# Performance work log

Hardware: AMD Instinct MI355X
Metric: run time of the kernel (lower is better)

The kernel has to match this reference:

```python
import jax, jax.numpy as jnp
import numpy as np

B, S, E, H = 2, 2048, 1024, 16
D = E // H


def setup_inputs() -> dict:
    key = jax.random.key(0)
    ks = jax.random.split(key, 12)
    init = lambda k, shp: (jax.random.normal(k, shp, dtype=jnp.float32) * 0.02)
    return {
        "q": jax.random.normal(ks[0], (B, S, E), dtype=jnp.float32),
        "k": jax.random.normal(ks[1], (B, S, E), dtype=jnp.float32),
        "v": jax.random.normal(ks[2], (B, S, E), dtype=jnp.float32),
        "wq": init(ks[3], (E, E)), "bq": jnp.zeros((E,), jnp.float32),
        "wk": init(ks[4], (E, E)), "bk": jnp.zeros((E,), jnp.float32),
        "wv": init(ks[5], (E, E)), "bv": jnp.zeros((E,), jnp.float32),
        "wo": init(ks[6], (E, E)), "bo": jnp.zeros((E,), jnp.float32),
        "gamma": jnp.ones((E,), jnp.float32),
        "beta": jnp.zeros((E,), jnp.float32),
        "mask": 1,
    }


def _split_heads(x):
    # [B,S,E] -> [B,H,S,D]
    return x.reshape(x.shape[0], x.shape[1], H, D).transpose(0, 2, 1, 3)


def _mha(q, k, v, wq, bq, wk, bk, wv, bv, wo, bo, gamma, beta, causal):
    residual = q
    query = _split_heads(q @ wq + bq)
    key = _split_heads(k @ wk + bk)
    value = _split_heads(v @ wv + bv)
    scale = jnp.sqrt(jnp.float32(D)) + 1e-8  # matches torch: sqrt(dk) + 1e-8
    score = jnp.einsum("bhqd,bhkd->bhqk", query, key) / scale
    if causal:
        cm = jnp.tril(jnp.ones((S, S), dtype=bool))  # 1 - triu(...,1)
        score = jnp.where(cm[None, None], score, -jnp.inf)
    attn = jax.nn.softmax(score, axis=-1)
    ctx = jnp.einsum("bhqk,bhkd->bhqd", attn, value)
    ctx = ctx.transpose(0, 2, 1, 3).reshape(ctx.shape[0], S, E)
    o = ctx @ wo + bo  # dropout is identity in eval mode
    x = residual + o
    mu = jnp.mean(x, axis=-1, keepdims=True)
    var = jnp.var(x, axis=-1, keepdims=True)
    return (x - mu) / jnp.sqrt(var + 1e-5) * gamma + beta


def reference(q, k, v, wq, bq, wk, bk, wv, bv, wo, bo, gamma, beta, mask):
    return _mha(q, k, v, wq, bq, wk, bk, wv, bv, wo, bo, gamma, beta, bool(mask))
```

## Files before the change

### kernel.cpp

```cpp
#include <hip/hip_runtime.h>
#include <hip/hip_bf16.h>

typedef __bf16 bf16x8 __attribute__((ext_vector_type(8)));
typedef __attribute__((ext_vector_type(8))) short short8_t;
typedef __attribute__((ext_vector_type(4))) short short4_t;
typedef __attribute__((ext_vector_type(4))) float f32x4;

#define DEV __device__ __forceinline__

constexpr int Bc = 2, Sc = 2048, Ec = 1024, Hc = 16, Dc = 64;
constexpr int Mc = Bc * Sc;
constexpr int NT = Sc / 64;
constexpr float kQS = (float)((1.0 / (8.0 + 1e-8)) * 1.4426950408889634);

DEV short f2bf(float f) {
  unsigned int u = __builtin_bit_cast(unsigned int, f);
  unsigned int r = u + 0x7fffu + ((u >> 16) & 1u);
  return (short)(r >> 16);
}
DEV short bfc(float f) { __bf16 h = (__bf16)f; return __builtin_bit_cast(short, h); }

DEV float fexp2(float x) {
#if __has_builtin(__builtin_amdgcn_exp2f)
  return __builtin_amdgcn_exp2f(x);
#else
  float r;
  asm("v_exp_f32 %0, %1" : "=v"(r) : "v"(x));
  return r;
#endif
}

DEV void gload16(const short* g, short* lds) {
  __builtin_amdgcn_global_load_lds((const __attribute__((address_space(1))) void*)g,
                                   (__attribute__((address_space(3))) void*)lds, 16, 0, 0);
}

struct Prep {
  const float* w[4]; short* wt[4];
  const float* x[3]; short* y[3];
};
__global__ __launch_bounds__(256) void k_prep(Prep a) {
  const int bid = blockIdx.x;
  if (bid < 4096) {
    __shared__ float tile[32][33];
    const int z = bid >> 10, bk = (bid >> 5) & 31, bn = bid & 31;
    const float* w = a.w[z];
    short* wt = a.wt[z];
    int tx = threadIdx.x & 31, ty = threadIdx.x >> 5;
#pragma unroll
    for (int i = 0; i < 4; i++)
      tile[ty + i * 8][tx] = w[(size_t)(bk * 32 + ty + i * 8) * Ec + bn * 32 + tx];
    __syncthreads();
#pragma unroll
    for (int i = 0; i < 4; i++)
      wt[(size_t)(bn * 32 + ty + i * 8) * Ec + bk * 32 + tx] = f2bf(tile[tx][ty + i * 8]);
  } else {
    const int idx = bid - 4096;
    const int z = idx >> 11, c = idx & 2047;
    const float* x = a.x[z];
    short* y = a.y[z];
    size_t i = ((size_t)c * 256 + threadIdx.x) * 8;
    float4 v0 = *(const float4*)(x + i);
    float4 v1 = *(const float4*)(x + i + 4);
    short8_t h;
    h[0] = bfc(v0.x); h[1] = bfc(v0.y); h[2] = bfc(v0.z); h[3] = bfc(v0.w);
    h[4] = bfc(v1.x); h[5] = bfc(v1.y); h[6] = bfc(v1.z); h[7] = bfc(v1.w);
    *(short8_t*)(y + i) = h;
  }
}

DEV void gemm_mfma(const short* lA, const short* lB, f32x4 (&acc)[4][4], int lane, int wm, int wn) {
#pragma unroll
  for (int kc = 0; kc < 2; kc++) {
    bf16x8 a[4], b[4];
#pragma unroll
    for (int mf = 0; mf < 4; mf++) {
      int row = wm * 64 + mf * 16 + (lane & 15);
      int ch = (kc * 4 + (lane >> 4)) ^ (row & 7);
      a[mf] = *(const bf16x8*)&lA[row * 64 + (ch << 3)];
    }
#pragma unroll
    for (int nf = 0; nf < 4; nf++) {
      int row = wn * 64 + nf * 16 + (lane & 15);
      int ch = (kc * 4 + (lane >> 4)) ^ (row & 7);
      b[nf] = *(const bf16x8*)&lB[row * 64 + (ch << 3)];
    }
#pragma unroll
    for (int mf = 0; mf < 4; mf++)
#pragma unroll
      for (int nf = 0; nf < 4; nf++)
        acc[mf][nf] = __builtin_amdgcn_mfma_f32_16x16x32_bf16(a[mf], b[nf], acc[mf][nf], 0, 0, 0);
  }
}

struct QKV3 { const short* A[3]; const short* Bt[3]; const float* bias[3]; short* out[3]; };

__global__ __launch_bounds__(256, 2) void k_gemm_qkv(QKV3 args) {
  __shared__ short lA[2][128 * 64];
  __shared__ short lB[2][128 * 64];
  int lin = blockIdx.x + 8 * blockIdx.y + 256 * blockIdx.z;
  lin = (lin & 7) * 96 + (lin >> 3);
  const int bx = lin & 7, by = (lin >> 3) & 31, z = lin >> 8;
  const short* A = args.A[z];
  const short* Bt = args.Bt[z];
  const float* bias = args.bias[z];
  short* out = args.out[z];
  const int t = threadIdx.x;
  const int m0 = by * 128, n0 = bx * 128;
  const int lane = t & 63, wid = t >> 6;
  const int wm = wid >> 1, wn = wid & 1;
  const int rl = lane >> 3, chs = ((lane & 7) ^ rl) << 3;

  f32x4 acc[4][4];
#pragma unroll
  for (int i = 0; i < 4; i++)
#pragma unroll
    for (int j = 0; j < 4; j++) acc[i][j] = {0.f, 0.f, 0.f, 0.f};

  auto stage = [&](int st, int buf) {
    const int k0 = st * 64;
#pragma unroll
    for (int j = 0; j < 4; j++) {
      int r0 = wid * 32 + j * 8;
      gload16(A + (size_t)(m0 + r0 + rl) * Ec + k0 + chs, &lA[buf][r0 * 64]);
      gload16(Bt + (size_t)(n0 + r0 + rl) * Ec + k0 + chs, &lB[buf][r0 * 64]);
    }
  };
  stage(0, 0);
  stage(1, 1);
  for (int s = 0; s < 15; s++) {
    asm volatile("s_waitcnt vmcnt(8)" ::: "memory");
    __builtin_amdgcn_s_barrier();
    gemm_mfma(lA[s & 1], lB[s & 1], acc, lane, wm, wn);
    __builtin_amdgcn_s_barrier();
    if (s + 2 < 16) stage(s + 2, s & 1);
  }
  asm volatile("s_waitcnt vmcnt(0)" ::: "memory");
  __builtin_amdgcn_s_barrier();
  gemm_mfma(lA[1], lB[1], acc, lane, wm, wn);

#pragma unroll
  for (int mf = 0; mf < 4; mf++) {
#pragma unroll
    for (int nf = 0; nf < 4; nf++) {
      int col = n0 + wn * 64 + nf * 16 + (lane & 15);
      float bs = bias[col];
      int row0 = m0 + wm * 64 + mf * 16 + ((lane >> 4) << 2);
      int bh = ((row0 >> 11) << 4) + (col >> 6);
      int d = col & 63;
      size_t bhbase = (size_t)bh * Sc * Dc;
      if (z == 0) {
#pragma unroll
        for (int r = 0; r < 4; r++) {
          int row = row0 + r;
          size_t off = bhbase + (size_t)(row & 2047) * Dc + d;
          out[off] = f2bf((acc[mf][nf][r] + bs) * kQS);
        }
      } else if (z == 1) {
#pragma unroll
        for (int r = 0; r < 4; r++) {
          int sr = (row0 + r) & 2047;
          size_t off = bhbase + (size_t)(sr >> 4) * 1024 + ((d >> 5) * 512) +
                       (((d >> 3) & 3) * 128) + ((sr & 15) * 8) + (d & 7);
          out[off] = f2bf(acc[mf][nf][r] + bs);
        }
      } else {
        short4_t h;
#pragma unroll
        for (int r = 0; r < 4; r++) h[r] = f2bf(acc[mf][nf][r] + bs);
        int s0 = row0 & 2047;
        size_t off = bhbase + (size_t)(s0 >> 6) * 4096 + (((s0 >> 5) & 1) * 2048) +
                     (((d >> 4) & 3) * 512) + ((((s0 >> 3) & 3) * 16 + (d & 15)) * 8) + (s0 & 7);
        *(short4_t*)&out[off] = h;
      }
    }
  }
}

__global__ __launch_bounds__(256, 2) void k_gemm_o(const short* __restrict__ A,
                                                   const short* __restrict__ Bt,
                                                   const float* __restrict__ bias,
                                                   const float* __restrict__ res,
                                                   float* __restrict__ out) {
  __shared__ short lA[2][128 * 64];
  __shared__ short lB[2][128 * 64];
  int lin = blockIdx.x + 8 * blockIdx.y;
  lin = (lin & 7) * 32 + (lin >> 3);
  const int bx = lin & 7, by = lin >> 3;
  const int t = threadIdx.x;
  const int m0 = by * 128, n0 = bx * 128;
  const int lane = t & 63, wid = t >> 6;
  const int wm = wid >> 1, wn = wid & 1;
  const int rl = lane >> 3, chs = ((lane & 7) ^ rl) << 3;

  f32x4 acc[4][4];
#pragma unroll
  for (int i = 0; i < 4; i++)
#pragma unroll
    for (int j = 0; j < 4; j++) acc[i][j] = {0.f, 0.f, 0.f, 0.f};

  auto stage = [&](int st, int buf) {
    const int k0 = st * 64;
#pragma unroll
    for (int j = 0; j < 4; j++) {
      int r0 = wid * 32 + j * 8;
      gload16(A + (size_t)(m0 + r0 + rl) * Ec + k0 + chs, &lA[buf][r0 * 64]);
      gload16(Bt + (size_t)(n0 + r0 + rl) * Ec + k0 + chs, &lB[buf][r0 * 64]);
    }
  };
  stage(0, 0);
  stage(1, 1);
  for (int s = 0; s < 15; s++) {
    asm volatile("s_waitcnt vmcnt(8)" ::: "memory");
    __builtin_amdgcn_s_barrier();
    gemm_mfma(lA[s & 1], lB[s & 1], acc, lane, wm, wn);
    __builtin_amdgcn_s_barrier();
    if (s + 2 < 16) stage(s + 2, s & 1);
  }
  asm volatile("s_waitcnt vmcnt(0)" ::: "memory");
  __builtin_amdgcn_s_barrier();
  gemm_mfma(lA[1], lB[1], acc, lane, wm, wn);

#pragma unroll
  for (int mf = 0; mf < 4; mf++) {
#pragma unroll
    for (int nf = 0; nf < 4; nf++) {
      int col = n0 + wn * 64 + nf * 16 + (lane & 15);
      float bs = bias[col];
#pragma unroll
      for (int r = 0; r < 4; r++) {
        int row = m0 + wm * 64 + mf * 16 + ((lane >> 4) << 2) + r;
        out[(size_t)row * Ec + col] = acc[mf][nf][r] + bs + res[(size_t)row * Ec + col];
      }
    }
  }
}

__global__ __launch_bounds__(256, 2) void k_attn8(const short* __restrict__ Qp,
                                                  const short* __restrict__ Kf,
                                                  const short* __restrict__ Vf,
                                                  const int* __restrict__ maskp,
                                                  short* __restrict__ ctx) {
  __shared__ short lP[64 * 64];
  const int lin = blockIdx.x;
  const int bh = lin & 31, qi = lin >> 5;
  const int qtA = qi, qtB = NT - 1 - qi;
  const int t = threadIdx.x, lane = t & 63, w = t >> 6;
  const int gs = lane >> 4, l15 = lane & 15;
  const bool causal = maskp[0] != 0;
  const int b = bh >> 4, h = bh & 15;
  const size_t base = (size_t)bh * Sc * Dc;
  const int ktend = causal ? qtB : (NT - 1);

  bf16x8 aqA[2], aqB[2];
  {
    const short* qpA = Qp + base + (size_t)(qtA * 64 + w * 16 + l15) * Dc + gs * 8;
    const short* qpB = Qp + base + (size_t)(qtB * 64 + w * 16 + l15) * Dc + gs * 8;
    aqA[0] = *(const bf16x8*)(qpA);
    aqA[1] = *(const bf16x8*)(qpA + 32);
    aqB[0] = *(const bf16x8*)(qpB);
    aqB[1] = *(const bf16x8*)(qpB + 32);
  }
  bf16x8 ones;
#pragma unroll
  for (int j = 0; j < 8; j++) ones[j] = (__bf16)1.0f;

  f32x4 oA[4], oB[4], lsA, lsB;
#pragma unroll
  for (int i = 0; i < 4; i++) {
    oA[i] = {0.f, 0.f, 0.f, 0.f};
    oB[i] = {0.f, 0.f, 0.f, 0.f};
  }
  lsA = {0.f, 0.f, 0.f, 0.f};
  lsB = {0.f, 0.f, 0.f, 0.f};

  const int prow = w * 16 + l15, pswz = l15 & 7;
  short* pw[4];
  const short* pr[2];
#pragma unroll
  for (int mf = 0; mf < 4; mf++)
    pw[mf] = &lP[prow * 64 + (((2 * mf + (gs >> 1)) ^ pswz) << 3) + (gs & 1) * 4];
#pragma unroll
  for (int kc = 0; kc < 2; kc++)
    pr[kc] = &lP[prow * 64 + (((kc * 4 + gs) ^ pswz) << 3)];

  const short* Kb = Kf + base + lane * 8;
  const short* Vb = Vf + base + lane * 8;
  const int qloc = w * 16 + l15;

  bf16x8 kA[2][4], kB[2][4];
#pragma unroll
  for (int mf = 0; mf < 4; mf++) {
    kA[0][mf] = *(const bf16x8*)(Kb + mf * 1024);
    kA[1][mf] = *(const bf16x8*)(Kb + mf * 1024 + 512);
  }

  int kt = 0;
  auto tilepass = [&](const bf16x8 (&kc_)[2][4], const bf16x8 (&vf)[2][4],
                      const bf16x8 (&aq)[2], f32x4 (&oacc)[4], f32x4& lsum, bool diag) {
    f32x4 s[4];
#pragma unroll
    for (int mf = 0; mf < 4; mf++) s[mf] = {0.f, 0.f, 0.f, 0.f};
    __builtin_amdgcn_s_setprio(1);
#pragma unroll
    for (int c2 = 0; c2 < 2; c2++)
#pragma unroll
      for (int mf = 0; mf < 4; mf++)
        s[mf] = __builtin_amdgcn_mfma_f32_16x16x32_bf16(kc_[c2][mf], aq[c2], s[mf], 0, 0, 0);
    __builtin_amdgcn_s_setprio(0);
    if (diag) {
#pragma unroll
      for (int mf = 0; mf < 4; mf++) {
        short4_t hh;
#pragma unroll
        for (int r = 0; r < 4; r++) {
          float p = fexp2(s[mf][r]);
          if ((mf * 16 + gs * 4 + r) > qloc) p = 0.f;
          hh[r] = bfc(p);
        }
        *(short4_t*)pw[mf] = hh;
      }
    } else {
#pragma unroll
      for (int mf = 0; mf < 4; mf++) {
        short4_t hh;
#pragma unroll
        for (int r = 0; r < 4; r++) hh[r] = bfc(fexp2(s[mf][r]));
        *(short4_t*)pw[mf] = hh;
      }
    }
    bf16x8 pa[2];
    pa[0] = *(const bf16x8*)pr[0];
    pa[1] = *(const bf16x8*)pr[1];
    __builtin_amdgcn_s_setprio(1);
#pragma unroll
    for (int c2 = 0; c2 < 2; c2++) {
      lsum = __builtin_amdgcn_mfma_f32_16x16x32_bf16(pa[c2], ones, lsum, 0, 0, 0);
#pragma unroll
      for (int df = 0; df < 4; df++)
        oacc[df] = __builtin_amdgcn_mfma_f32_16x16x32_bf16(pa[c2], vf[c2][df], oacc[df], 0, 0, 0);
    }
    __builtin_amdgcn_s_setprio(0);
  };

  auto body = [&](bf16x8 (&kc_)[2][4], bf16x8 (&kn_)[2][4]) {
    if (kt < ktend) {
      const short* kp = Kb + (kt + 1) * 4096;
#pragma unroll
      for (int mf = 0; mf < 4; mf++) {
        kn_[0][mf] = *(const bf16x8*)(kp + mf * 1024);
        kn_[1][mf] = *(const bf16x8*)(kp + mf * 1024 + 512);
      }
    }
    const short* vp = Vb + kt * 4096;
    bf16x8 vf[2][4];
#pragma unroll
    for (int c2 = 0; c2 < 2; c2++)
#pragma unroll
      for (int df = 0; df < 4; df++)
        vf[c2][df] = *(const bf16x8*)(vp + c2 * 2048 + df * 512);
    __builtin_amdgcn_sched_barrier(0);

    tilepass(kc_, vf, aqB, oB, lsB, causal && (kt == qtB));
    if (!causal || (kt <= qtA))
      tilepass(kc_, vf, aqA, oA, lsA, causal && (kt == qtA));
  };

  while (true) {
    body(kA, kB);
    if (++kt > ktend) break;
    body(kB, kA);
    if (++kt > ktend) break;
  }

#pragma unroll
  for (int r = 0; r < 4; r++) {
    float ibB = 1.0f / lsB[r];
    float ibA = 1.0f / lsA[r];
    int srB = qtB * 64 + w * 16 + (gs << 2) + r;
    int srA = qtA * 64 + w * 16 + (gs << 2) + r;
#pragma unroll
    for (int df = 0; df < 4; df++) {
      int col = h * 64 + df * 16 + l15;
      ctx[(size_t)(b * Sc + srB) * Ec + col] = f2bf(oB[df][r] * ibB);
      ctx[(size_t)(b * Sc + srA) * Ec + col] = f2bf(oA[df][r] * ibA);
    }
  }
}

__global__ __launch_bounds__(256) void k_ln(float* __restrict__ x,
                                            const float* __restrict__ gamma,
                                            const float* __restrict__ beta) {
  int row = blockIdx.x, t = threadIdx.x;
  float4 v = *(const float4*)(x + (size_t)row * Ec + t * 4);
  float s = v.x + v.y + v.z + v.w;
  float sq = v.x * v.x + v.y * v.y + v.z * v.z + v.w * v.w;
#pragma unroll
  for (int m = 1; m < 64; m <<= 1) {
    s += __shfl_xor(s, m);
    sq += __shfl_xor(sq, m);
  }
  __shared__ float red[8];
  if ((t & 63) == 0) {
    red[t >> 6] = s;
    red[4 + (t >> 6)] = sq;
  }
  __syncthreads();
  s = red[0] + red[1] + red[2] + red[3];
  sq = red[4] + red[5] + red[6] + red[7];
  float mu = s * (1.f / Ec);
  float var = sq * (1.f / Ec) - mu * mu;
  float rstd = rsqrtf(var + 1e-5f);
  float4 g = *(const float4*)(gamma + t * 4);
  float4 bb = *(const float4*)(beta + t * 4);
  v.x = (v.x - mu) * rstd * g.x + bb.x;
  v.y = (v.y - mu) * rstd * g.y + bb.y;
  v.z = (v.z - mu) * rstd * g.z + bb.z;
  v.w = (v.w - mu) * rstd * g.w + bb.w;
  *(float4*)(x + (size_t)row * Ec + t * 4) = v;
}

extern "C" void kernel_launch(void* const* d_in, const int* in_sizes, int n_in,
                              void* d_out, int out_size, void* d_ws, size_t ws_size,
                              hipStream_t stream) {
  const float* q = (const float*)d_in[0];
  const float* k = (const float*)d_in[1];
  const float* v = (const float*)d_in[2];
  const float* wq = (const float*)d_in[3];
  const float* bq = (const float*)d_in[4];
  const float* wk = (const float*)d_in[5];
  const float* bk = (const float*)d_in[6];
  const float* wv = (const float*)d_in[7];
  const float* bv = (const float*)d_in[8];
  const float* wo = (const float*)d_in[9];
  const float* bo = (const float*)d_in[10];
  const float* gamma = (const float*)d_in[11];
  const float* beta = (const float*)d_in[12];
  const int* maskp = (const int*)d_in[13];
  float* out = (float*)d_out;

  short* wtq = (short*)d_ws;
  short* wtk = wtq + (size_t)Ec * Ec;
  short* wtv = wtk + (size_t)Ec * Ec;
  short* wto = wtv + (size_t)Ec * Ec;
  short* Qp = wto + (size_t)Ec * Ec;
  short* Kf = Qp + (size_t)Mc * Ec;
  short* Vf = Kf + (size_t)Mc * Ec;
  short* ctx = Vf + (size_t)Mc * Ec;

  short* xq = (short*)d_out;
  short* xk = xq + (size_t)Mc * Ec;
  short* xv = ctx;

  dim3 tb(256);

  Prep pargs;
  pargs.w[0] = wq; pargs.w[1] = wk; pargs.w[2] = wv; pargs.w[3] = wo;
  pargs.wt[0] = wtq; pargs.wt[1] = wtk; pargs.wt[2] = wtv; pargs.wt[3] = wto;
  pargs.x[0] = q; pargs.x[1] = k; pargs.x[2] = v;
  pargs.y[0] = xq; pargs.y[1] = xk; pargs.y[2] = xv;
  k_prep<<<dim3(4096 + 3 * (Mc * Ec / 2048)), tb, 0, stream>>>(pargs);

  QKV3 gargs;
  gargs.A[0] = xq; gargs.A[1] = xk; gargs.A[2] = xv;
  gargs.Bt[0] = wtq; gargs.Bt[1] = wtk; gargs.Bt[2] = wtv;
  gargs.bias[0] = bq; gargs.bias[1] = bk; gargs.bias[2] = bv;
  gargs.out[0] = Qp; gargs.out[1] = Kf; gargs.out[2] = Vf;
  k_gemm_qkv<<<dim3(Ec / 128, Mc / 128, 3), tb, 0, stream>>>(gargs);

  k_attn8<<<dim3(NT / 2 * Bc * Hc), tb, 0, stream>>>(Qp, Kf, Vf, maskp, ctx);

  k_gemm_o<<<dim3(Ec / 128, Mc / 128), tb, 0, stream>>>(ctx, wto, bo, q, out);

  k_ln<<<dim3(Mc), tb, 0, stream>>>(out, gamma, beta);
}
```

Before: 116.3 us.

## Fuse fp32-to-bf16 activation conversion into QKV GEMM and prefetch V tiles

The separate prep pass that converted q/k/v to bf16 is removed. The QKV GEMM now loads fp32 A rows into registers, converts them to bf16 and writes swizzled LDS tiles, using a register double buffer and a deeper vmcnt pipeline. This removes one full write and read of the activations but moves A loads off the direct global-to-LDS path and raises register pressure. Separately, the attention kernel now double-buffers V fragments, loading the next tile's V alongside K instead of loading the current tile's V right before use.

After: 201.1 us. +72.8%, slower.

```diff
diff --git a/kernel.cpp b/kernel.cpp
--- a/kernel.cpp
+++ b/kernel.cpp
@@ -35,38 +35,21 @@
                                    (__attribute__((address_space(3))) void*)lds, 16, 0, 0);
 }
 
-struct Prep {
-  const float* w[4]; short* wt[4];
-  const float* x[3]; short* y[3];
-};
+struct Prep { const float* w[4]; short* wt[4]; };
 __global__ __launch_bounds__(256) void k_prep(Prep a) {
+  __shared__ float tile[32][33];
   const int bid = blockIdx.x;
-  if (bid < 4096) {
-    __shared__ float tile[32][33];
-    const int z = bid >> 10, bk = (bid >> 5) & 31, bn = bid & 31;
-    const float* w = a.w[z];
-    short* wt = a.wt[z];
-    int tx = threadIdx.x & 31, ty = threadIdx.x >> 5;
-#pragma unroll
-    for (int i = 0; i < 4; i++)
-      tile[ty + i * 8][tx] = w[(size_t)(bk * 32 + ty + i * 8) * Ec + bn * 32 + tx];
-    __syncthreads();
-#pragma unroll
-    for (int i = 0; i < 4; i++)
-      wt[(size_t)(bn * 32 + ty + i * 8) * Ec + bk * 32 + tx] = f2bf(tile[tx][ty + i * 8]);
-  } else {
-    const int idx = bid - 4096;
-    const int z = idx >> 11, c = idx & 2047;
-    const float* x = a.x[z];
-    short* y = a.y[z];
-    size_t i = ((size_t)c * 256 + threadIdx.x) * 8;
-    float4 v0 = *(const float4*)(x + i);
-    float4 v1 = *(const float4*)(x + i + 4);
-    short8_t h;
-    h[0] = bfc(v0.x); h[1] = bfc(v0.y); h[2] = bfc(v0.z); h[3] = bfc(v0.w);
-    h[4] = bfc(v1.x); h[5] = bfc(v1.y); h[6] = bfc(v1.z); h[7] = bfc(v1.w);
-    *(short8_t*)(y + i) = h;
-  }
+  const int z = bid >> 10, bk = (bid >> 5) & 31, bn = bid & 31;
+  const float* w = a.w[z];
+  short* wt = a.wt[z];
+  int tx = threadIdx.x & 31, ty = threadIdx.x >> 5;
+#pragma unroll
+  for (int i = 0; i < 4; i++)
+    tile[ty + i * 8][tx] = w[(size_t)(bk * 32 + ty + i * 8) * Ec + bn * 32 + tx];
+  __syncthreads();
+#pragma unroll
+  for (int i = 0; i < 4; i++)
+    wt[(size_t)(bn * 32 + ty + i * 8) * Ec + bk * 32 + tx] = f2bf(tile[tx][ty + i * 8]);
 }
 
 DEV void gemm_mfma(const short* lA, const short* lB, f32x4 (&acc)[4][4], int lane, int wm, int wn) {
@@ -93,7 +76,7 @@
   }
 }
 
-struct QKV3 { const short* A[3]; const short* Bt[3]; const float* bias[3]; short* out[3]; };
+struct QKV3 { const float* A[3]; const short* Bt[3]; const float* bias[3]; short* out[3]; };
 
 __global__ __launch_bounds__(256, 2) void k_gemm_qkv(QKV3 args) {
   __shared__ short lA[2][128 * 64];
@@ -101,7 +84,7 @@
   int lin = blockIdx.x + 8 * blockIdx.y + 256 * blockIdx.z;
   lin = (lin & 7) * 96 + (lin >> 3);
   const int bx = lin & 7, by = (lin >> 3) & 31, z = lin >> 8;
-  const short* A = args.A[z];
+  const float* A = args.A[z];
   const short* Bt = args.Bt[z];
   const float* bias = args.bias[z];
   short* out = args.out[z];
@@ -110,6 +93,10 @@
   const int lane = t & 63, wid = t >> 6;
   const int wm = wid >> 1, wn = wid & 1;
   const int rl = lane >> 3, chs = ((lane & 7) ^ rl) << 3;
+  const int arow = t >> 1, ahalf = t & 1, aswz = arow & 7;
+  const float* Arow = A + (size_t)(m0 + arow) * Ec + ahalf * 32;
+  short* const awp = &lA[0][arow * 64];
+  const size_t abufstride = 128 * 64;
 
   f32x4 acc[4][4];
 #pragma unroll
@@ -117,27 +104,65 @@
 #pragma unroll
     for (int j = 0; j < 4; j++) acc[i][j] = {0.f, 0.f, 0.f, 0.f};
 
-  auto stage = [&](int st, int buf) {
+  float4 rAa[8], rAb[8];
+  auto loadA = [&](int st, float4 (&r)[8]) {
+    const float* ap = Arow + st * 64;
+#pragma unroll
+    for (int j = 0; j < 8; j++) r[j] = *(const float4*)(ap + j * 4);
+  };
+  auto writeA = [&](int st, float4 (&r)[8]) {
+    short* aw = awp + (st & 1) * abufstride;
+#pragma unroll
+    for (int j = 0; j < 4; j++) {
+      short8_t h;
+      h[0] = bfc(r[2 * j].x); h[1] = bfc(r[2 * j].y);
+      h[2] = bfc(r[2 * j].z); h[3] = bfc(r[2 * j].w);
+      h[4] = bfc(r[2 * j + 1].x); h[5] = bfc(r[2 * j + 1].y);
+      h[6] = bfc(r[2 * j + 1].z); h[7] = bfc(r[2 * j + 1].w);
+      *(short8_t*)&aw[((ahalf * 4 + j) ^ aswz) << 3] = h;
+    }
+  };
+  auto stageB = [&](int st, int buf) {
     const int k0 = st * 64;
 #pragma unroll
     for (int j = 0; j < 4; j++) {
       int r0 = wid * 32 + j * 8;
-      gload16(A + (size_t)(m0 + r0 + rl) * Ec + k0 + chs, &lA[buf][r0 * 64]);
       gload16(Bt + (size_t)(n0 + r0 + rl) * Ec + k0 + chs, &lB[buf][r0 * 64]);
     }
   };
-  stage(0, 0);
-  stage(1, 1);
-  for (int s = 0; s < 15; s++) {
-    asm volatile("s_waitcnt vmcnt(8)" ::: "memory");
+
+  loadA(0, rAa);
+  loadA(1, rAb);
+  __builtin_amdgcn_sched_barrier(0);
+  writeA(0, rAa);
+  loadA(2, rAa);
+  stageB(0, 0);
+  __builtin_amdgcn_sched_barrier(0);
+  writeA(1, rAb);
+  loadA(3, rAb);
+  stageB(1, 1);
+  asm volatile("s_waitcnt lgkmcnt(0)" ::: "memory");
+
+  auto iter = [&](int s, float4 (&rc)[8]) {
     __builtin_amdgcn_s_barrier();
     gemm_mfma(lA[s & 1], lB[s & 1], acc, lane, wm, wn);
     __builtin_amdgcn_s_barrier();
-    if (s + 2 < 16) stage(s + 2, s & 1);
-  }
+    if (s + 2 < 16) writeA(s + 2, rc);
+    if (s + 4 < 16) loadA(s + 4, rc);
+    if (s + 2 < 16) stageB(s + 2, s & 1);
+    asm volatile("s_waitcnt lgkmcnt(0)" ::: "memory");
+  };
+
+  for (int s = 0; s <= 12; s++) {
+    asm volatile("s_waitcnt vmcnt(12)" ::: "memory");
+    if (s & 1) iter(s, rAb); else iter(s, rAa);
+  }
+  asm volatile("s_waitcnt vmcnt(4)" ::: "memory");
+  iter(13, rAb);
+  asm volatile("s_waitcnt vmcnt(4)" ::: "memory");
+  iter(14, rAa);
   asm volatile("s_waitcnt vmcnt(0)" ::: "memory");
-  __builtin_amdgcn_s_barrier();
-  gemm_mfma(lA[1], lB[1], acc, lane, wm, wn);
+  iter(15, rAb);
 
 #pragma unroll
   for (int mf = 0; mf < 4; mf++) {
@@ -236,7 +261,7 @@
   }
 }
 
-__global__ __launch_bounds__(256, 2) void k_attn8(const short* __restrict__ Qp,
+__global__ __launch_bounds__(256, 2) void k_attn9(const short* __restrict__ Qp,
                                                   const short* __restrict__ Kf,
                                                   const short* __restrict__ Vf,
                                                   const int* __restrict__ maskp,
@@ -288,15 +313,20 @@
   const short* Vb = Vf + base + lane * 8;
   const int qloc = w * 16 + l15;
 
-  bf16x8 kA[2][4], kB[2][4];
+  bf16x8 kA[2][4], kB[2][4], vA[2][4], vB[2][4];
 #pragma unroll
   for (int mf = 0; mf < 4; mf++) {
     kA[0][mf] = *(const bf16x8*)(Kb + mf * 1024);
     kA[1][mf] = *(const bf16x8*)(Kb + mf * 1024 + 512);
   }
+#pragma unroll
+  for (int c2 = 0; c2 < 2; c2++)
+#pragma unroll
+    for (int df = 0; df < 4; df++)
+      vA[c2][df] = *(const bf16x8*)(Vb + c2 * 2048 + df * 512);
 
   int kt = 0;
-  auto tilepass = [&](const bf16x8 (&kc_)[2][4], const bf16x8 (&vf)[2][4],
+  auto tilepass = [&](const bf16x8 (&kc_)[2][4], const bf16x8 (&vc_)[2][4],
                       const bf16x8 (&aq)[2], f32x4 (&oacc)[4], f32x4& lsum, bool diag) {
     f32x4 s[4];
 #pragma unroll
@@ -338,38 +368,38 @@
       lsum = __builtin_amdgcn_mfma_f32_16x16x32_bf16(pa[c2], ones, lsum, 0, 0, 0);
 #pragma unroll
       for (int df = 0; df < 4; df++)
-        oacc[df] = __builtin_amdgcn_mfma_f32_16x16x32_bf16(pa[c2], vf[c2][df], oacc[df], 0, 0, 0);
+        oacc[df] = __builtin_amdgcn_mfma_f32_16x16x32_bf16(pa[c2], vc_[c2][df], oacc[df], 0, 0, 0);
     }
     __builtin_amdgcn_s_setprio(0);
   };
 
-  auto body = [&](bf16x8 (&kc_)[2][4], bf16x8 (&kn_)[2][4]) {
+  auto body = [&](bf16x8 (&kc_)[2][4], bf16x8 (&kn_)[2][4],
+                  bf16x8 (&vc_)[2][4], bf16x8 (&vn_)[2][4]) {
     if (kt < ktend) {
       const short* kp = Kb + (kt + 1) * 4096;
+      const short* vp = Vb + (kt + 1) * 4096;
 #pragma unroll
       for (int mf = 0; mf < 4; mf++) {
         kn_[0][mf] = *(const bf16x8*)(kp + mf * 1024);
         kn_[1][mf] = *(const bf16x8*)(kp + mf * 1024 + 512);
       }
-    }
-    const short* vp = Vb + kt * 4096;
-    bf16x8 vf[2][4];
-#pragma unroll
-    for (int c2 = 0; c2 < 2; c2++)
-#pragma unroll
-      for (int df = 0; df < 4; df++)
-        vf[c2][df] = *(const bf16x8*)(vp + c2 * 2048 + df * 512);
+#pragma unroll
+      for (int c2 = 0; c2 < 2; c2++)
+#pragma unroll
+        for (int df = 0; df < 4; df++)
+          vn_[c2][df] = *(const bf16x8*)(vp + c2 * 2048 + df * 512);
+    }
     __builtin_amdgcn_sched_barrier(0);
 
-    tilepass(kc_, vf, aqB, oB, lsB, causal && (kt == qtB));
+    tilepass(kc_, vc_, aqB, oB, lsB, causal && (kt == qtB));
     if (!causal || (kt <= qtA))
-      tilepass(kc_, vf, aqA, oA, lsA, causal && (kt == qtA));
+      tilepass(kc_, vc_, aqA, oA, lsA, causal && (kt == qtA));
   };
 
   while (true) {
-    body(kA, kB);
+    body(kA, kB, vA, vB);
     if (++kt > ktend) break;
-    body(kB, kA);
+    body(kB, kA, vB, vA);
     if (++kt > ktend) break;
   }
 
@@ -448,27 +478,21 @@
   short* Vf = Kf + (size_t)Mc * Ec;
   short* ctx = Vf + (size_t)Mc * Ec;
 
-  short* xq = (short*)d_out;
-  short* xk = xq + (size_t)Mc * Ec;
-  short* xv = ctx;
-
   dim3 tb(256);
 
   Prep pargs;
   pargs.w[0] = wq; pargs.w[1] = wk; pargs.w[2] = wv; pargs.w[3] = wo;
   pargs.wt[0] = wtq; pargs.wt[1] = wtk; pargs.wt[2] = wtv; pargs.wt[3] = wto;
-  pargs.x[0] = q; pargs.x[1] = k; pargs.x[2] = v;
-  pargs.y[0] = xq; pargs.y[1] = xk; pargs.y[2] = xv;
-  k_prep<<<dim3(4096 + 3 * (Mc * Ec / 2048)), tb, 0, stream>>>(pargs);
+  k_prep<<<dim3(4096), tb, 0, stream>>>(pargs);
 
   QKV3 gargs;
-  gargs.A[0] = xq; gargs.A[1] = xk; gargs.A[2] = xv;
+  gargs.A[0] = q; gargs.A[1] = k; gargs.A[2] = v;
   gargs.Bt[0] = wtq; gargs.Bt[1] = wtk; gargs.Bt[2] = wtv;
   gargs.bias[0] = bq; gargs.bias[1] = bk; gargs.bias[2] = bv;
   gargs.out[0] = Qp; gargs.out[1] = Kf; gargs.out[2] = Vf;
   k_gemm_qkv<<<dim3(Ec / 128, Mc / 128, 3), tb, 0, stream>>>(gargs);
 
-  k_attn8<<<dim3(NT / 2 * Bc * Hc), tb, 0, stream>>>(Qp, Kf, Vf, maskp, ctx);
+  k_attn9<<<dim3(NT / 2 * Bc * Hc), tb, 0, stream>>>(Qp, Kf, Vf, maskp, ctx);
 
   k_gemm_o<<<dim3(Ec / 128, Mc / 128), tb, 0, stream>>>(ctx, wto, bo, q, out);
 
```
